# Optimization experiments

Measured on AMD Instinct MI355X. Metric: run time of the kernel, lower is better.

Reference implementation:

```python
import jax, jax.numpy as jnp
import numpy as np

C = 1024   # n_embd = dim_att = dim_k = dim_v
H = 16     # n_head
K = 64     # k_head_size
V = 64     # v_head_size
DF = 2048  # dim_ffn = (2*C)//32*32
B = 4
T = 1024
N_LAYER = 24
LAYER_ID = 12


def setup_inputs() -> dict:
    key = jax.random.key(0)
    ks = jax.random.split(key, 8)
    r01 = LAYER_ID / (N_LAYER - 1)
    r10 = 1.0 - LAYER_ID / N_LAYER
    ddd = (jnp.arange(C, dtype=jnp.float32) / C)[None, None, :]
    maa_x = 1.0 - ddd ** r10
    maa_k = 1.0 - ddd ** r10
    maa_v = 1.0 - (ddd ** r10 + 0.3 * r01)
    maa_r = 1.0 - ddd ** (0.5 * r10)
    n = jnp.arange(C, dtype=jnp.float32)
    zigzag = ((jnp.arange(C) + 1) % 3 - 1).astype(jnp.float32) * 0.1
    u = (r01 * (1.0 - n / (C - 1)) + zigzag).reshape(H, K)
    # LoRA mats: torch init is zeros / uniform(-0.01,0.01); use small uniform for both
    # so the token-shift LoRA path is actually exercised.
    w1 = jax.random.uniform(ks[0], (C, 96), minval=-0.01, maxval=0.01)
    w2 = jax.random.uniform(ks[1], (3, 32, C), minval=-0.01, maxval=0.01)
    s = 0.02
    Wr = jax.random.normal(ks[2], (C, C)) * s
    Wk = jax.random.normal(ks[3], (C, C)) * s
    Wvg = jax.random.normal(ks[4], (C, 2 * (C + DF))) * s
    Wo = jax.random.normal(ks[5], (C + DF, C)) * s
    ln_g = jnp.ones((C,), jnp.float32)
    ln_b = jnp.zeros((C,), jnp.float32)
    x = jax.random.normal(ks[6], (B, T, C), dtype=jnp.float32)
    return dict(x=x, maa_x=maa_x, maa_k=maa_k, maa_v=maa_v, maa_r=maa_r,
                w1=w1, w2=w2, u=u, Wr=Wr, Wk=Wk, Wvg=Wvg, Wo=Wo,
                ln_g=ln_g, ln_b=ln_b)


def _wkv6(r, k, v, e, u):
    # r,k,e: (B,T,H,K); v: (B,T,H,V); u: (H,K). Decayed linear-attention scan.
    rt = r.transpose(1, 0, 2, 3)
    kt = k.transpose(1, 0, 2, 3)
    vt = v.transpose(1, 0, 2, 3)
    et = e.transpose(1, 0, 2, 3)

    def step(S, inp):  # S: (B,H,K,V)
        r_t, k_t, v_t, e_t = inp
        kv = k_t[..., :, None] * v_t[..., None, :]           # (B,H,K,V)
        out = jnp.einsum('bhk,bhkv->bhv', r_t, S + u[None, :, :, None] * kv)
        return S * e_t[..., :, None] + kv, out

    S0 = jnp.zeros((r.shape[0], u.shape[0], u.shape[1], v.shape[-1]), r.dtype)
    _, o = jax.lax.scan(step, S0, (rt, kt, vt, et))
    return o.transpose(1, 0, 2, 3)  # (B,T,H,V)


def reference(x, maa_x, maa_k, maa_v, maa_r, w1, w2, u, Wr, Wk, Wvg, Wo, ln_g, ln_b):
    Bx, Tx, Cx = x.shape
    # time_shift: ZeroPad2d((0,0,1,-1)) -> shift right by 1 along T with zero pad
    xs = jnp.concatenate([jnp.zeros_like(x[:, :1]), x[:, :-1]], axis=1)
    xx = xs - x
    xxx = x + xx * maa_x
    m = jnp.tanh(xxx @ w1).reshape(Bx, Tx, 3, -1)        # (B,T,3,32)
    m = jnp.einsum('btld,ldc->lbtc', m, w2)              # (3,B,T,C)
    mk, mv, mr = m[0], m[1], m[2]
    xk = x + xx * (maa_k + mk)
    xv = x + xx * (maa_v + mv)
    xr = x + xx * (maa_r + mr)
    r = xr @ Wr
    w = xk @ Wk
    e = jnp.exp(-jnp.exp(w))   # per-channel decay used by the WKV kernel
    k = 1.0 - e                # k = 1 - exp(-exp(w))
    vg = xv @ Wvg
    vffn, gate = jnp.split(vg, 2, axis=-1)
    vffn = vffn * jax.nn.silu(gate)
    v, ffn = vffn[..., :Cx], vffn[..., Cx:]
    o = _wkv6(r.reshape(Bx, Tx, H, K), k.reshape(Bx, Tx, H, K),
              v.reshape(Bx, Tx, H, V), e.reshape(Bx, Tx, H, K), u)
    o = o.reshape(Bx, Tx, Cx)
    mu = o.mean(-1, keepdims=True)
    var = o.var(-1, keepdims=True)
    o = (o - mu) / jnp.sqrt(var + 1e-5) * ln_g + ln_b
    return jnp.concatenate([o, ffn], axis=-1) @ Wo
```

## Files before the change

kernel.cpp:

```cpp
#include <hip/hip_runtime.h>
#include <hip/hip_bf16.h>
#include <math.h>

#define Bn 4
#define Tn 1024
#define Cn 1024
#define Hn 16
#define Kn 64
#define DFn 2048
#define NCn 16
#define Ln 64

typedef __bf16 bf16x8 __attribute__((ext_vector_type(8)));
typedef float f32x4 __attribute__((ext_vector_type(4)));

#define GLD(dst, src) \
  __builtin_amdgcn_global_load_lds((__attribute__((address_space(1))) const void*)(src), \
                                   (__attribute__((address_space(3))) void*)(dst), 16, 0, 0)

__device__ __forceinline__ float rdlane(float v, int l) {
  return __int_as_float(__builtin_amdgcn_readlane(__float_as_int(v), l));
}

__device__ __forceinline__ unsigned short bfbits(float f) {
  union { __hip_bfloat16 h; unsigned short u; } cv;
  cv.h = __float2bfloat16(f);
  return cv.u;
}

__global__ __launch_bounds__(256) void k_setup(const float* __restrict__ w1,
                                               const float* __restrict__ w2,
                                               const float* __restrict__ Wr,
                                               const float* __restrict__ Wk,
                                               const float* __restrict__ Wvg,
                                               const float* __restrict__ Wo,
                                               const float* __restrict__ x,
                                               const float* __restrict__ maa_x,
                                               __hip_bfloat16* __restrict__ w1t,
                                               __hip_bfloat16* __restrict__ w2t,
                                               __hip_bfloat16* __restrict__ Wrt,
                                               __hip_bfloat16* __restrict__ Wkt,
                                               __hip_bfloat16* __restrict__ Wvgt,
                                               __hip_bfloat16* __restrict__ Wot,
                                               float* __restrict__ xx,
                                               __hip_bfloat16* __restrict__ xxx16) {
  int b = blockIdx.x;
  if (b >= 11456) {
    int idx = (b - 11456) * 256 + threadIdx.x;
    int c4 = idx & 255;
    int bt = idx >> 8;
    int t = bt & (Tn - 1);
    const float4* x4 = (const float4*)x;
    float4 xv = x4[idx];
    float4 xp;
    if (t > 0) xp = x4[idx - 256];
    else { xp.x = 0.f; xp.y = 0.f; xp.z = 0.f; xp.w = 0.f; }
    float4 d;
    d.x = xp.x - xv.x; d.y = xp.y - xv.y; d.z = xp.z - xv.z; d.w = xp.w - xv.w;
    float4 m = ((const float4*)maa_x)[c4];
    ushort4 o;
    o.x = bfbits(fmaf(d.x, m.x, xv.x));
    o.y = bfbits(fmaf(d.y, m.y, xv.y));
    o.z = bfbits(fmaf(d.z, m.z, xv.z));
    o.w = bfbits(fmaf(d.w, m.w, xv.w));
    ((float4*)xx)[idx] = d;
    ((ushort4*)xxx16)[idx] = o;
    return;
  }
  const float* W; __hip_bfloat16* Wt; int K, N, nx, rel;
  if (b < 96)        { W = w1;  Wt = w1t;  K = 1024; N = 96;   nx = 3;   rel = b; }
  else if (b < 192)  { int l = (b - 96) >> 5; rel = (b - 96) & 31;
                       W = w2 + l * 32768; Wt = w2t + l * 32768; K = 32; N = 1024; nx = 32; }
  else if (b < 1216) { W = Wr;  Wt = Wrt;  K = 1024; N = 1024; nx = 32;  rel = b - 192; }
  else if (b < 2240) { W = Wk;  Wt = Wkt;  K = 1024; N = 1024; nx = 32;  rel = b - 1216; }
  else if (b < 8384) { W = Wvg; Wt = Wvgt; K = 1024; N = 6144; nx = 192; rel = b - 2240; }
  else               { W = Wo;  Wt = Wot;  K = 3072; N = 1024; nx = 32;  rel = b - 8384; }
  int n0 = (rel % nx) * 32, k0 = (rel / nx) * 32;
  __shared__ float tile[32][33];
  int tid = threadIdx.x;
  int c = tid & 31, r = tid >> 5;
  #pragma unroll
  for (int i = 0; i < 4; ++i)
    tile[r + i * 8][c] = W[(size_t)(k0 + r + i * 8) * N + n0 + c];
  __syncthreads();
  #pragma unroll
  for (int i = 0; i < 4; ++i)
    Wt[(size_t)(n0 + r + i * 8) * K + k0 + c] = __float2bfloat16(tile[c][r + i * 8]);
}

__global__ __launch_bounds__(256) void k_mix1_16(const __hip_bfloat16* __restrict__ A,
                                                 const __hip_bfloat16* __restrict__ Bt,
                                                 __hip_bfloat16* __restrict__ m1) {
  const int K = 1024;
  __shared__ __align__(16) __hip_bfloat16 Al[128 * 32];
  __shared__ __align__(16) __hip_bfloat16 Bl[96 * 32];
  const int tid = threadIdx.x;
  const int wid = tid >> 6, lane = tid & 63;
  const int wr = wid >> 1, wc = wid & 1;
  const int row0 = blockIdx.x * 128;
  const char* gsrc[4];
  char* ldst[4];
  bool act[4];
  #pragma unroll
  for (int i = 0; i < 4; ++i) {
    const int s = i * 4 + wid;
    act[i] = (s < 14);
    const int ss = act[i] ? s : 0;
    if (ss < 8) {
      const int r = ss * 16 + (lane >> 2);
      gsrc[i] = (const char*)(A + (size_t)(row0 + r) * K) + (lane & 3) * 16;
      ldst[i] = (char*)&Al[0] + ss * 1024;
    } else {
      const int r = (ss - 8) * 16 + (lane >> 2);
      gsrc[i] = (const char*)(Bt + (size_t)r * K) + (lane & 3) * 16;
      ldst[i] = (char*)&Bl[0] + (ss - 8) * 1024;
    }
  }
  f32x4 acc[4][3];
  #pragma unroll
  for (int i = 0; i < 4; ++i)
    #pragma unroll
    for (int j = 0; j < 3; ++j)
      acc[i][j] = (f32x4){0.f, 0.f, 0.f, 0.f};
  const int g = lane >> 4, m = lane & 15;
  for (int k0 = 0; k0 < K; k0 += 32) {
    #pragma unroll
    for (int i = 0; i < 4; ++i) if (act[i]) GLD(ldst[i], gsrc[i]);
    #pragma unroll
    for (int i = 0; i < 4; ++i) gsrc[i] += 64;
    __syncthreads();
    bf16x8 af[4], bfr[3];
    #pragma unroll
    for (int i = 0; i < 4; ++i)
      af[i] = *(const bf16x8*)&Al[(wr * 64 + i * 16 + m) * 32 + g * 8];
    #pragma unroll
    for (int j = 0; j < 3; ++j)
      bfr[j] = *(const bf16x8*)&Bl[(wc * 48 + j * 16 + m) * 32 + g * 8];
    #pragma unroll
    for (int i = 0; i < 4; ++i)
      #pragma unroll
      for (int j = 0; j < 3; ++j)
        acc[i][j] = __builtin_amdgcn_mfma_f32_16x16x32_bf16(af[i], bfr[j], acc[i][j], 0, 0, 0);
    __syncthreads();
  }
  #pragma unroll
  for (int i = 0; i < 4; ++i) {
    const int grow = row0 + wr * 64 + i * 16 + g * 4;
    #pragma unroll
    for (int j = 0; j < 3; ++j) {
      const int gcol = wc * 48 + j * 16 + m;
      #pragma unroll
      for (int e = 0; e < 4; ++e)
        m1[(size_t)(grow + e) * 96 + gcol] = __float2bfloat16(tanhf(acc[i][j][e]));
    }
  }
}

__global__ __launch_bounds__(256) void k_mix2_16(const __hip_bfloat16* __restrict__ m1,
                                                 const __hip_bfloat16* __restrict__ w2t,
                                                 const float* __restrict__ x,
                                                 const float* __restrict__ xx,
                                                 const float* __restrict__ maa_k,
                                                 const float* __restrict__ maa_v,
                                                 const float* __restrict__ maa_r,
                                                 __hip_bfloat16* __restrict__ xk,
                                                 __hip_bfloat16* __restrict__ xv,
                                                 __hip_bfloat16* __restrict__ xr) {
  __shared__ __align__(16) __hip_bfloat16 Al[128 * 96];
  __shared__ __align__(16) __hip_bfloat16 Bl[3 * 64 * 32];
  const int tid = threadIdx.x;
  const int wid = tid >> 6, lane = tid & 63;
  const int wr = wid >> 1, wc = wid & 1;
  const int row0 = blockIdx.y * 128, col0 = blockIdx.x * 64;
  {
    const char* abase = (const char*)(m1 + (size_t)row0 * 96) + lane * 16;
    #pragma unroll
    for (int i = 0; i < 6; ++i) {
      const int s = wid + i * 4;
      GLD((char*)&Al[0] + s * 1024, abase + s * 1024);
    }
  }
  {
    const char* bbase = (const char*)w2t + (size_t)col0 * 64 + lane * 16;
    #pragma unroll
    for (int i = 0; i < 3; ++i) {
      const int s = wid + i * 4;
      const int l = s >> 2, q = s & 3;
      GLD((char*)&Bl[0] + s * 1024, bbase + (size_t)l * 65536 + q * 1024);
    }
  }
  __syncthreads();
  const int g = lane >> 4, m = lane & 15;
  f32x4 a0[4][2], a1[4][2], a2[4][2];
  #pragma unroll
  for (int i = 0; i < 4; ++i)
    #pragma unroll
    for (int j = 0; j < 2; ++j) {
      a0[i][j] = (f32x4){0.f,0.f,0.f,0.f};
      a1[i][j] = (f32x4){0.f,0.f,0.f,0.f};
      a2[i][j] = (f32x4){0.f,0.f,0.f,0.f};
    }
  #pragma unroll
  for (int l = 0; l < 3; ++l) {
    bf16x8 af[4], bfj[2];
    #pragma unroll
    for (int i = 0; i < 4; ++i)
      af[i] = *(const bf16x8*)&Al[(wr * 64 + i * 16 + m) * 96 + l * 32 + g * 8];
    #pragma unroll
    for (int j = 0; j < 2; ++j)
      bfj[j] = *(const bf16x8*)&Bl[(l * 64 + wc * 32 + j * 16 + m) * 32 + g * 8];
    #pragma unroll
    for (int i = 0; i < 4; ++i)
      #pragma unroll
      for (int j = 0; j < 2; ++j) {
        if (l == 0) a0[i][j] = __builtin_amdgcn_mfma_f32_16x16x32_bf16(af[i], bfj[j], a0[i][j], 0, 0, 0);
        if (l == 1) a1[i][j] = __builtin_amdgcn_mfma_f32_16x16x32_bf16(af[i], bfj[j], a1[i][j], 0, 0, 0);
        if (l == 2) a2[i][j] = __builtin_amdgcn_mfma_f32_16x16x32_bf16(af[i], bfj[j], a2[i][j], 0, 0, 0);
      }
  }
  #pragma unroll
  for (int i = 0; i < 4; ++i) {
    const int grow = row0 + wr * 64 + i * 16 + g * 4;
    #pragma unroll
    for (int j = 0; j < 2; ++j) {
      const int gcol = col0 + wc * 32 + j * 16 + m;
      const float mk_ = maa_k[gcol], mv_ = maa_v[gcol], mr_ = maa_r[gcol];
      #pragma unroll
      for (int e = 0; e < 4; ++e) {
        const size_t off = (size_t)(grow + e) * 1024 + gcol;
        const float xval = x[off], xxv = xx[off];
        xk[off] = __float2bfloat16(fmaf(xxv, mk_ + a0[i][j][e], xval));
        xv[off] = __float2bfloat16(fmaf(xxv, mv_ + a1[i][j][e], xval));
        xr[off] = __float2bfloat16(fmaf(xxv, mr_ + a2[i][j][e], xval));
      }
    }
  }
}

__global__ __launch_bounds__(256) void k_gemm_re(const __hip_bfloat16* __restrict__ Ar,
                                                 const __hip_bfloat16* __restrict__ Btr,
                                                 float* __restrict__ Cr,
                                                 const __hip_bfloat16* __restrict__ Ak,
                                                 const __hip_bfloat16* __restrict__ Btk,
                                                 float* __restrict__ Ck) {
  const int K = 1024, N = 1024;
  const int z = blockIdx.z;
  const __hip_bfloat16* A  = z ? Ak : Ar;
  const __hip_bfloat16* Bt = z ? Btk : Btr;
  float* C = z ? Ck : Cr;
  __shared__ __align__(16) __hip_bfloat16 Al[128 * 32];
  __shared__ __align__(16) __hip_bfloat16 Bl[64 * 32];
  const int tid = threadIdx.x;
  const int wid = tid >> 6, lane = tid & 63;
  const int wr = wid >> 1, wc = wid & 1;
  const int row0 = blockIdx.y * 128, col0 = blockIdx.x * 64;
  const char* gsrc[3];
  char* ldst[3];
  #pragma unroll
  for (int i = 0; i < 3; ++i) {
    const int s = wid + i * 4;
    if (s < 8) {
      const int r = s * 16 + (lane >> 2);
      gsrc[i] = (const char*)(A + (size_t)(row0 + r) * K) + (lane & 3) * 16;
      ldst[i] = (char*)&Al[0] + s * 1024;
    } else {
      const int r = (s - 8) * 16 + (lane >> 2);
      gsrc[i] = (const char*)(Bt + (size_t)(col0 + r) * K) + (lane & 3) * 16;
      ldst[i] = (char*)&Bl[0] + (s - 8) * 1024;
    }
  }
  f32x4 acc[4][2];
  #pragma unroll
  for (int i = 0; i < 4; ++i)
    #pragma unroll
    for (int j = 0; j < 2; ++j)
      acc[i][j] = (f32x4){0.f, 0.f, 0.f, 0.f};
  const int g = lane >> 4, m = lane & 15;
  for (int k0 = 0; k0 < K; k0 += 32) {
    #pragma unroll
    for (int i = 0; i < 3; ++i) GLD(ldst[i], gsrc[i]);
    #pragma unroll
    for (int i = 0; i < 3; ++i) gsrc[i] += 64;
    __syncthreads();
    bf16x8 af[4], bfr[2];
    #pragma unroll
    for (int i = 0; i < 4; ++i)
      af[i] = *(const bf16x8*)&Al[(wr * 64 + i * 16 + m) * 32 + g * 8];
    #pragma unroll
    for (int j = 0; j < 2; ++j)
      bfr[j] = *(const bf16x8*)&Bl[(wc * 32 + j * 16 + m) * 32 + g * 8];
    #pragma unroll
    for (int i = 0; i < 4; ++i)
      #pragma unroll
      for (int j = 0; j < 2; ++j)
        acc[i][j] = __builtin_amdgcn_mfma_f32_16x16x32_bf16(af[i], bfr[j], acc[i][j], 0, 0, 0);
    __syncthreads();
  }
  #pragma unroll
  for (int i = 0; i < 4; ++i) {
    const int grow = row0 + wr * 64 + i * 16 + g * 4;
    #pragma unroll
    for (int j = 0; j < 2; ++j) {
      const int gcol = col0 + wc * 32 + j * 16 + m;
      #pragma unroll
      for (int e = 0; e < 4; ++e) {
        float val = acc[i][j][e];
        if (z) val = expf(-expf(val));
        C[(size_t)(grow + e) * N + gcol] = val;
      }
    }
  }
}

__global__ __launch_bounds__(256) void k_gemm_vg16(const __hip_bfloat16* __restrict__ A,
                                                   const __hip_bfloat16* __restrict__ Bt,
                                                   float* __restrict__ v,
                                                   __hip_bfloat16* __restrict__ ffn) {
  const int K = 1024;
  __shared__ __align__(16) __hip_bfloat16 Al[128 * 32];
  __shared__ __align__(16) __hip_bfloat16 B1l[64 * 32];
  __shared__ __align__(16) __hip_bfloat16 B2l[64 * 32];
  const int tid = threadIdx.x;
  const int wid = tid >> 6, lane = tid & 63;
  const int wr = wid >> 1, wc = wid & 1;
  const int row0 = blockIdx.y * 128, col0 = blockIdx.x * 64;
  const char* gsrc[4];
  char* ldst[4];
  #pragma unroll
  for (int i = 0; i < 4; ++i) {
    const int s = wid + i * 4;
    if (s < 8) {
      const int r = s * 16 + (lane >> 2);
      gsrc[i] = (const char*)(A + (size_t)(row0 + r) * K) + (lane & 3) * 16;
      ldst[i] = (char*)&Al[0] + s * 1024;
    } else if (s < 12) {
      const int r = col0 + (s - 8) * 16 + (lane >> 2);
      gsrc[i] = (const char*)(Bt + (size_t)r * K) + (lane & 3) * 16;
      ldst[i] = (char*)&B1l[0] + (s - 8) * 1024;
    } else {
      const int r = 3072 + col0 + (s - 12) * 16 + (lane >> 2);
      gsrc[i] = (const char*)(Bt + (size_t)r * K) + (lane & 3) * 16;
      ldst[i] = (char*)&B2l[0] + (s - 12) * 1024;
    }
  }
  f32x4 a1[4][2], a2[4][2];
  #pragma unroll
  for (int i = 0; i < 4; ++i)
    #pragma unroll
    for (int j = 0; j < 2; ++j) {
      a1[i][j] = (f32x4){0.f, 0.f, 0.f, 0.f};
      a2[i][j] = (f32x4){0.f, 0.f, 0.f, 0.f};
    }
  const int g = lane >> 4, m = lane & 15;
  for (int k0 = 0; k0 < K; k0 += 32) {
    #pragma unroll
    for (int i = 0; i < 4; ++i) GLD(ldst[i], gsrc[i]);
    #pragma unroll
    for (int i = 0; i < 4; ++i) gsrc[i] += 64;
    __syncthreads();
    bf16x8 af[4], b1f[2], b2f[2];
    #pragma unroll
    for (int i = 0; i < 4; ++i)
      af[i] = *(const bf16x8*)&Al[(wr * 64 + i * 16 + m) * 32 + g * 8];
    #pragma unroll
    for (int j = 0; j < 2; ++j) {
      b1f[j] = *(const bf16x8*)&B1l[(wc * 32 + j * 16 + m) * 32 + g * 8];
      b2f[j] = *(const bf16x8*)&B2l[(wc * 32 + j * 16 + m) * 32 + g * 8];
    }
    #pragma unroll
    for (int i = 0; i < 4; ++i)
      #pragma unroll
      for (int j = 0; j < 2; ++j) {
        a1[i][j] = __builtin_amdgcn_mfma_f32_16x16x32_bf16(af[i], b1f[j], a1[i][j], 0, 0, 0);
        a2[i][j] = __builtin_amdgcn_mfma_f32_16x16x32_bf16(af[i], b2f[j], a2[i][j], 0, 0, 0);
      }
    __syncthreads();
  }
  const bool to_v = (col0 < 1024);
  #pragma unroll
  for (int i = 0; i < 4; ++i) {
    const int grow = row0 + wr * 64 + i * 16 + g * 4;
    #pragma unroll
    for (int j = 0; j < 2; ++j) {
      const int gcol = col0 + wc * 32 + j * 16 + m;
      #pragma unroll
      for (int e = 0; e < 4; ++e) {
        float gate = a2[i][j][e];
        float val = a1[i][j][e] * (gate / (1.f + expf(-gate)));
        if (to_v) v[(size_t)(grow + e) * 1024 + gcol] = val;
        else ffn[(size_t)(grow + e) * 2048 + (gcol - 1024)] = __float2bfloat16(val);
      }
    }
  }
}

__global__ __launch_bounds__(256) void k_gemm_wo16(const __hip_bfloat16* __restrict__ A1,
                                                   const __hip_bfloat16* __restrict__ A2,
                                                   const __hip_bfloat16* __restrict__ Bt,
                                                   float* __restrict__ C) {
  const int Kt = 3072;
  __shared__ __align__(16) __hip_bfloat16 Al[128 * 32];
  __shared__ __align__(16) __hip_bfloat16 Bl[64 * 32];
  const int tid = threadIdx.x;
  const int wid = tid >> 6, lane = tid & 63;
  const int wr = wid >> 1, wc = wid & 1;
  const int row0 = blockIdx.y * 128, col0 = blockIdx.x * 64;
  const char* gsrc[3];
  char* ldst[3];
  #pragma unroll
  for (int i = 0; i < 3; ++i) {
    const int s = wid + i * 4;
    if (s < 8) {
      const int r = s * 16 + (lane >> 2);
      gsrc[i] = (const char*)(A1 + (size_t)(row0 + r) * 1024) + (lane & 3) * 16;
      ldst[i] = (char*)&Al[0] + s * 1024;
    } else {
      const int r = col0 + (s - 8) * 16 + (lane >> 2);
      gsrc[i] = (const char*)(Bt + (size_t)r * Kt) + (lane & 3) * 16;
      ldst[i] = (char*)&Bl[0] + (s - 8) * 1024;
    }
  }
  f32x4 acc[4][2];
  #pragma unroll
  for (int i = 0; i < 4; ++i)
    #pragma unroll
    for (int j = 0; j < 2; ++j)
      acc[i][j] = (f32x4){0.f, 0.f, 0.f, 0.f};
  const int g = lane >> 4, m = lane & 15;

  #define WO_STEP() do {                                                          \
    _Pragma("unroll")                                                             \
    for (int i = 0; i < 3; ++i) GLD(ldst[i], gsrc[i]);                            \
    _Pragma("unroll")                                                             \
    for (int i = 0; i < 3; ++i) gsrc[i] += 64;                                    \
    __syncthreads();                                                              \
    bf16x8 af[4], bfr[2];                                                         \
    _Pragma("unroll")                                                             \
    for (int i = 0; i < 4; ++i)                                                   \
      af[i] = *(const bf16x8*)&Al[(wr * 64 + i * 16 + m) * 32 + g * 8];           \
    _Pragma("unroll")                                                             \
    for (int j = 0; j < 2; ++j)                                                   \
      bfr[j] = *(const bf16x8*)&Bl[(wc * 32 + j * 16 + m) * 32 + g * 8];          \
    _Pragma("unroll")                                                             \
    for (int i = 0; i < 4; ++i)                                                   \
      _Pragma("unroll")                                                           \
      for (int j = 0; j < 2; ++j)                                                 \
        acc[i][j] = __builtin_amdgcn_mfma_f32_16x16x32_bf16(af[i], bfr[j],        \
                                                            acc[i][j], 0, 0, 0); \
    __syncthreads();                                                              \
  } while (0)

  for (int k0 = 0; k0 < 1024; k0 += 32) WO_STEP();
  #pragma unroll
  for (int i = 0; i < 3; ++i) {
    const int s = wid + i * 4;
    if (s < 8) {
      const int r = s * 16 + (lane >> 2);
      gsrc[i] = (const char*)(A2 + (size_t)(row0 + r) * 2048) + (lane & 3) * 16;
    }
  }
  for (int k0 = 0; k0 < 2048; k0 += 32) WO_STEP();
  #undef WO_STEP

  #pragma unroll
  for (int i = 0; i < 4; ++i) {
    const int grow = row0 + wr * 64 + i * 16 + g * 4;
    #pragma unroll
    for (int j = 0; j < 2; ++j) {
      const int gcol = col0 + wc * 32 + j * 16 + m;
      #pragma unroll
      for (int e = 0; e < 4; ++e)
        C[(size_t)(grow + e) * 1024 + gcol] = acc[i][j][e];
    }
  }
}

#define TTn 8
__global__ __launch_bounds__(256) void k_wkv1(const float* __restrict__ r,
                                              const float* __restrict__ e,
                                              const float* __restrict__ v,
                                              const float* __restrict__ u,
                                              float* __restrict__ o,
                                              float* __restrict__ Dcum,
                                              float* __restrict__ Dtot,
                                              float* __restrict__ Inc) {
  int blk = blockIdx.x;
  int c = blk & (NCn - 1);
  int bh = blk >> 4;
  int b = bh >> 4, h = bh & 15;
  int tid = threadIdx.x, wave = tid >> 6, lane = tid & 63;
  size_t base = (size_t)b * Tn * Cn + (size_t)h * 64 + (size_t)c * Ln * Cn;
  int jbase = wave * 16 + (lane & 15);
  float uv = u[h * 64 + jbase];
  float st[16];
  #pragma unroll
  for (int i = 0; i < 16; ++i) st[i] = 0.f;
  float cum = 1.f;
  __shared__ float yp[4][TTn][64];
  for (int tb = 0; tb < Ln / TTn; ++tb) {
    float rv8[TTn], ev8[TTn], vv8[TTn];
    #pragma unroll
    for (int tt = 0; tt < TTn; ++tt) {
      size_t off = base + (size_t)(tb * TTn + tt) * Cn;
      rv8[tt] = r[off + jbase];
      ev8[tt] = e[off + jbase];
      vv8[tt] = v[off + lane];
    }
    float yb[TTn];
    #pragma unroll
    for (int tt = 0; tt < TTn; ++tt) {
      const float rv = rv8[tt], ev = ev8[tt], vv = vv8[tt];
      if (lane < 16)
        Dcum[base + (size_t)(tb * TTn + tt) * Cn + jbase] = cum;
      cum *= ev;
      float p = rv * uv * (1.f - ev);
      p += __shfl_xor(p, 1, 16);
      p += __shfl_xor(p, 2, 16);
      p += __shfl_xor(p, 4, 16);
      p += __shfl_xor(p, 8, 16);
      float y = p * vv;
      #pragma unroll
      for (int jj = 0; jj < 16; ++jj) {
        float rj = rdlane(rv, jj);
        float ej = rdlane(ev, jj);
        float kv = fmaf(-ej, vv, vv);
        y = fmaf(rj, st[jj], y);
        st[jj] = fmaf(st[jj], ej, kv);
      }
      yb[tt] = y;
    }
    #pragma unroll
    for (int tt = 0; tt < TTn; ++tt) yp[wave][tt][lane] = yb[tt];
    __syncthreads();
    #pragma unroll
    for (int q = 0; q < TTn / 4; ++q) {
      int tt = wave * (TTn / 4) + q;
      size_t off = base + (size_t)(tb * TTn + tt) * Cn;
      o[off + lane] = yp[0][tt][lane] + yp[1][tt][lane] + yp[2][tt][lane] + yp[3][tt][lane];
    }
    __syncthreads();
  }
  size_t sbase = ((size_t)bh * NCn + c) * 4096;
  #pragma unroll
  for (int jj = 0; jj < 16; ++jj)
    Inc[sbase + (size_t)(wave * 16 + jj) * 64 + lane] = st[jj];
  if (lane < 16)
    Dtot[((size_t)bh * NCn + c) * 64 + jbase] = cum;
}

__global__ __launch_bounds__(256) void k_wkv2(float* __restrict__ S,
                                              const float* __restrict__ Dtot) {
  int bh = blockIdx.x;
  int tid = threadIdx.x;
  float4 s[4];
  #pragma unroll
  for (int j = 0; j < 4; ++j) { s[j].x = 0.f; s[j].y = 0.f; s[j].z = 0.f; s[j].w = 0.f; }
  size_t sb = (size_t)bh * NCn * 4096;
  for (int c = 0; c < NCn; ++c) {
    float4* entry = (float4*)(S + sb + (size_t)c * 4096);
    const float* dt = Dtot + ((size_t)bh * NCn + c) * 64;
    #pragma unroll
    for (int j = 0; j < 4; ++j) {
      int idx4 = tid + j * 256;
      int k = idx4 >> 4;
      float d = dt[k];
      float4 inc = entry[idx4];
      float4 cur = s[j];
      entry[idx4] = cur;
      s[j].x = fmaf(cur.x, d, inc.x);
      s[j].y = fmaf(cur.y, d, inc.y);
      s[j].z = fmaf(cur.z, d, inc.z);
      s[j].w = fmaf(cur.w, d, inc.w);
    }
  }
}

__global__ __launch_bounds__(256) void k_wkv3(const float* __restrict__ r,
                                              const float* __restrict__ Dcum,
                                              const float* __restrict__ S,
                                              float* __restrict__ o) {
  int blk = blockIdx.x;
  int c = blk & (NCn - 1);
  if (c == 0) return;
  int bh = blk >> 4;
  int b = bh >> 4, h = bh & 15;
  int tid = threadIdx.x, wave = tid >> 6, lane = tid & 63;
  const float* Sg = S + ((size_t)bh * NCn + c) * 4096;
  float sreg[64];
  #pragma unroll
  for (int k = 0; k < 64; ++k) sreg[k] = Sg[k * 64 + lane];
  size_t base = (size_t)b * Tn * Cn + (size_t)h * 64 + (size_t)c * Ln * Cn;
  for (int ti = 0; ti < 16; ++ti) {
    int t = wave * 16 + ti;
    size_t off = base + (size_t)t * Cn;
    float rd = r[off + lane] * Dcum[off + lane];
    float y = 0.f;
    #pragma unroll
    for (int k = 0; k < 64; ++k)
      y = fmaf(rdlane(rd, k), sreg[k], y);
    o[off + lane] += y;
  }
}

__global__ __launch_bounds__(256) void k_ln(const float* __restrict__ o,
                                            const float* __restrict__ g,
                                            const float* __restrict__ bta,
                                            __hip_bfloat16* __restrict__ ln16) {
  int bt = blockIdx.x, tid = threadIdx.x;
  const float4* row = (const float4*)(o + (size_t)bt * 1024);
  float4 v = row[tid];
  float s = v.x + v.y + v.z + v.w;
  float s2 = fmaf(v.x, v.x, fmaf(v.y, v.y, fmaf(v.z, v.z, v.w * v.w)));
  #pragma unroll
  for (int m = 1; m < 64; m <<= 1) {
    s += __shfl_xor(s, m, 64);
    s2 += __shfl_xor(s2, m, 64);
  }
  __shared__ float rs[4], rq[4];
  if ((tid & 63) == 0) { rs[tid >> 6] = s; rq[tid >> 6] = s2; }
  __syncthreads();
  s = rs[0] + rs[1] + rs[2] + rs[3];
  s2 = rq[0] + rq[1] + rq[2] + rq[3];
  float mu = s * (1.f / 1024.f);
  float var = s2 * (1.f / 1024.f) - mu * mu;
  float rstd = rsqrtf(var + 1e-5f);
  float4 gv = ((const float4*)g)[tid];
  float4 bv = ((const float4*)bta)[tid];
  ushort4 outv;
  outv.x = bfbits(fmaf((v.x - mu) * rstd, gv.x, bv.x));
  outv.y = bfbits(fmaf((v.y - mu) * rstd, gv.y, bv.y));
  outv.z = bfbits(fmaf((v.z - mu) * rstd, gv.z, bv.z));
  outv.w = bfbits(fmaf((v.w - mu) * rstd, gv.w, bv.w));
  ((ushort4*)((unsigned short*)ln16 + (size_t)bt * 1024))[tid] = outv;
}

extern "C" void kernel_launch(void* const* d_in, const int* in_sizes, int n_in,
                              void* d_out, int out_size, void* d_ws, size_t ws_size,
                              hipStream_t stream) {
  const float* x     = (const float*)d_in[0];
  const float* maa_x = (const float*)d_in[1];
  const float* maa_k = (const float*)d_in[2];
  const float* maa_v = (const float*)d_in[3];
  const float* maa_r = (const float*)d_in[4];
  const float* w1    = (const float*)d_in[5];
  const float* w2    = (const float*)d_in[6];
  const float* u     = (const float*)d_in[7];
  const float* Wr    = (const float*)d_in[8];
  const float* Wk    = (const float*)d_in[9];
  const float* Wvg   = (const float*)d_in[10];
  const float* Wo    = (const float*)d_in[11];
  const float* ln_g  = (const float*)d_in[12];
  const float* ln_b  = (const float*)d_in[13];
  float* out = (float*)d_out;
  float* ws = (float*)d_ws;

  const size_t M1 = 1048576;
  float* xx    = ws;
  __hip_bfloat16* xxx16 = (__hip_bfloat16*)(ws + 4 * M1);
  __hip_bfloat16* m1_16 = (__hip_bfloat16*)(ws + 8 * M1);
  __hip_bfloat16* w1t = (__hip_bfloat16*)(ws + 8 * M1 + 393216);
  __hip_bfloat16* w2t = (__hip_bfloat16*)(ws + 8 * M1 + 442368);
  __hip_bfloat16* xk16 = (__hip_bfloat16*)(ws + 8 * M1 + 524288);
  __hip_bfloat16* xv16 = (__hip_bfloat16*)(ws + 10 * M1 + 524288);
  __hip_bfloat16* xr16 = (__hip_bfloat16*)(ws + 12 * M1 + 524288);
  float* ee    = ws + 14 * M1 + 524288;
  float* vv    = ws + 18 * M1 + 524288;
  float* Sbuf  = ws + 22 * M1 + 524288;
  __hip_bfloat16* ffn16 = (__hip_bfloat16*)(ws + 26 * M1 + 524288);
  __hip_bfloat16* Wr16t = (__hip_bfloat16*)(ws + 30 * M1 + 524288);
  __hip_bfloat16* Wk16t = (__hip_bfloat16*)(ws + 31 * M1);
  __hip_bfloat16* Wvg16t = (__hip_bfloat16*)(ws + 31 * M1 + 524288);
  __hip_bfloat16* Wo16t = (__hip_bfloat16*)(ws + 34 * M1 + 524288);
  float* rr = ws + 4 * M1;
  float* oo = xx;
  float* Dcum = ws + 8 * M1 + 524288;
  float* Dtot = (float*)m1_16;
  __hip_bfloat16* ln16 = (__hip_bfloat16*)Sbuf;

  k_setup<<<15552, 256, 0, stream>>>(w1, w2, Wr, Wk, Wvg, Wo, x, maa_x,
                                     w1t, w2t, Wr16t, Wk16t, Wvg16t, Wo16t,
                                     xx, xxx16);
  k_mix1_16<<<32, 256, 0, stream>>>(xxx16, w1t, m1_16);
  k_mix2_16<<<dim3(16, 32), 256, 0, stream>>>(m1_16, w2t, x, xx, maa_k, maa_v, maa_r,
                                              xk16, xv16, xr16);
  k_gemm_re<<<dim3(16, 32, 2), 256, 0, stream>>>(xr16, Wr16t, rr, xk16, Wk16t, ee);
  k_gemm_vg16<<<dim3(48, 32), 256, 0, stream>>>(xv16, Wvg16t, vv, ffn16);
  k_wkv1<<<64 * NCn, 256, 0, stream>>>(rr, ee, vv, u, oo, Dcum, Dtot, Sbuf);
  k_wkv2<<<64, 256, 0, stream>>>(Sbuf, Dtot);
  k_wkv3<<<64 * NCn, 256, 0, stream>>>(rr, Dcum, Sbuf, oo);
  k_ln<<<4096, 256, 0, stream>>>(oo, ln_g, ln_b, ln16);
  k_gemm_wo16<<<dim3(16, 32), 256, 0, stream>>>(ln16, ffn16, Wo16t, out);
}
```

Measured before the change: 322.8 us.

## Merge r/k and vg GEMMs into one launch; load wkv scalars via uniform loads

The separate r/k GEMM and value-gate GEMM launches are combined into a single 2560-block kernel that picks its sub-problem from the block index. This removes one launch and the tail gap between the two GEMMs, letting both sets of tiles share the GPU at once. In the wkv1 scan, the per-step readlane broadcasts of r and e are replaced by loads through a wave-uniform address, which the compiler can turn into scalar loads that take VALU pressure off the inner loop. The risks are extra scalar-memory latency in the serial recurrence, and an uneven mix of block sizes in the merged grid.

```diff
diff --git a/kernel.cpp b/kernel.cpp
--- a/kernel.cpp
+++ b/kernel.cpp
@@ -237,93 +237,92 @@
   }
 }
 
-__global__ __launch_bounds__(256) void k_gemm_re(const __hip_bfloat16* __restrict__ Ar,
-                                                 const __hip_bfloat16* __restrict__ Btr,
-                                                 float* __restrict__ Cr,
-                                                 const __hip_bfloat16* __restrict__ Ak,
-                                                 const __hip_bfloat16* __restrict__ Btk,
-                                                 float* __restrict__ Ck) {
-  const int K = 1024, N = 1024;
-  const int z = blockIdx.z;
-  const __hip_bfloat16* A  = z ? Ak : Ar;
-  const __hip_bfloat16* Bt = z ? Btk : Btr;
-  float* C = z ? Ck : Cr;
-  __shared__ __align__(16) __hip_bfloat16 Al[128 * 32];
-  __shared__ __align__(16) __hip_bfloat16 Bl[64 * 32];
-  const int tid = threadIdx.x;
-  const int wid = tid >> 6, lane = tid & 63;
-  const int wr = wid >> 1, wc = wid & 1;
-  const int row0 = blockIdx.y * 128, col0 = blockIdx.x * 64;
-  const char* gsrc[3];
-  char* ldst[3];
-  #pragma unroll
-  for (int i = 0; i < 3; ++i) {
-    const int s = wid + i * 4;
-    if (s < 8) {
-      const int r = s * 16 + (lane >> 2);
-      gsrc[i] = (const char*)(A + (size_t)(row0 + r) * K) + (lane & 3) * 16;
-      ldst[i] = (char*)&Al[0] + s * 1024;
-    } else {
-      const int r = (s - 8) * 16 + (lane >> 2);
-      gsrc[i] = (const char*)(Bt + (size_t)(col0 + r) * K) + (lane & 3) * 16;
-      ldst[i] = (char*)&Bl[0] + (s - 8) * 1024;
-    }
-  }
-  f32x4 acc[4][2];
-  #pragma unroll
-  for (int i = 0; i < 4; ++i)
-    #pragma unroll
-    for (int j = 0; j < 2; ++j)
-      acc[i][j] = (f32x4){0.f, 0.f, 0.f, 0.f};
-  const int g = lane >> 4, m = lane & 15;
-  for (int k0 = 0; k0 < K; k0 += 32) {
-    #pragma unroll
-    for (int i = 0; i < 3; ++i) GLD(ldst[i], gsrc[i]);
-    #pragma unroll
-    for (int i = 0; i < 3; ++i) gsrc[i] += 64;
-    __syncthreads();
-    bf16x8 af[4], bfr[2];
-    #pragma unroll
-    for (int i = 0; i < 4; ++i)
-      af[i] = *(const bf16x8*)&Al[(wr * 64 + i * 16 + m) * 32 + g * 8];
-    #pragma unroll
-    for (int j = 0; j < 2; ++j)
-      bfr[j] = *(const bf16x8*)&Bl[(wc * 32 + j * 16 + m) * 32 + g * 8];
-    #pragma unroll
-    for (int i = 0; i < 4; ++i)
-      #pragma unroll
-      for (int j = 0; j < 2; ++j)
-        acc[i][j] = __builtin_amdgcn_mfma_f32_16x16x32_bf16(af[i], bfr[j], acc[i][j], 0, 0, 0);
-    __syncthreads();
-  }
-  #pragma unroll
-  for (int i = 0; i < 4; ++i) {
-    const int grow = row0 + wr * 64 + i * 16 + g * 4;
-    #pragma unroll
-    for (int j = 0; j < 2; ++j) {
-      const int gcol = col0 + wc * 32 + j * 16 + m;
-      #pragma unroll
-      for (int e = 0; e < 4; ++e) {
-        float val = acc[i][j][e];
-        if (z) val = expf(-expf(val));
-        C[(size_t)(grow + e) * N + gcol] = val;
-      }
-    }
-  }
-}
-
-__global__ __launch_bounds__(256) void k_gemm_vg16(const __hip_bfloat16* __restrict__ A,
-                                                   const __hip_bfloat16* __restrict__ Bt,
-                                                   float* __restrict__ v,
-                                                   __hip_bfloat16* __restrict__ ffn) {
+__global__ __launch_bounds__(256) void k_gemm_rev(const __hip_bfloat16* __restrict__ xr,
+                                                  const __hip_bfloat16* __restrict__ Wrt,
+                                                  float* __restrict__ rr,
+                                                  const __hip_bfloat16* __restrict__ xk,
+                                                  const __hip_bfloat16* __restrict__ Wkt,
+                                                  float* __restrict__ ee,
+                                                  const __hip_bfloat16* __restrict__ xv,
+                                                  const __hip_bfloat16* __restrict__ Wvgt,
+                                                  float* __restrict__ vv,
+                                                  __hip_bfloat16* __restrict__ ffn) {
   const int K = 1024;
   __shared__ __align__(16) __hip_bfloat16 Al[128 * 32];
   __shared__ __align__(16) __hip_bfloat16 B1l[64 * 32];
   __shared__ __align__(16) __hip_bfloat16 B2l[64 * 32];
+  const int b = blockIdx.x;
   const int tid = threadIdx.x;
   const int wid = tid >> 6, lane = tid & 63;
   const int wr = wid >> 1, wc = wid & 1;
-  const int row0 = blockIdx.y * 128, col0 = blockIdx.x * 64;
+  const int g = lane >> 4, m = lane & 15;
+
+  if (b < 1024) {
+    const int z = b >> 9;
+    const int idx = b & 511;
+    const int row0 = (idx >> 4) * 128, col0 = (idx & 15) * 64;
+    const __hip_bfloat16* A  = z ? xk : xr;
+    const __hip_bfloat16* Bt = z ? Wkt : Wrt;
+    float* C = z ? ee : rr;
+    const char* gsrc[3];
+    char* ldst[3];
+    #pragma unroll
+    for (int i = 0; i < 3; ++i) {
+      const int s = wid + i * 4;
+      if (s < 8) {
+        const int r = s * 16 + (lane >> 2);
+        gsrc[i] = (const char*)(A + (size_t)(row0 + r) * K) + (lane & 3) * 16;
+        ldst[i] = (char*)&Al[0] + s * 1024;
+      } else {
+        const int r = (s - 8) * 16 + (lane >> 2);
+        gsrc[i] = (const char*)(Bt + (size_t)(col0 + r) * K) + (lane & 3) * 16;
+        ldst[i] = (char*)&B1l[0] + (s - 8) * 1024;
+      }
+    }
+    f32x4 acc[4][2];
+    #pragma unroll
+    for (int i = 0; i < 4; ++i)
+      #pragma unroll
+      for (int j = 0; j < 2; ++j)
+        acc[i][j] = (f32x4){0.f, 0.f, 0.f, 0.f};
+    for (int k0 = 0; k0 < K; k0 += 32) {
+      #pragma unroll
+      for (int i = 0; i < 3; ++i) GLD(ldst[i], gsrc[i]);
+      #pragma unroll
+      for (int i = 0; i < 3; ++i) gsrc[i] += 64;
+      __syncthreads();
+      bf16x8 af[4], bfr[2];
+      #pragma unroll
+      for (int i = 0; i < 4; ++i)
+        af[i] = *(const bf16x8*)&Al[(wr * 64 + i * 16 + m) * 32 + g * 8];
+      #pragma unroll
+      for (int j = 0; j < 2; ++j)
+        bfr[j] = *(const bf16x8*)&B1l[(wc * 32 + j * 16 + m) * 32 + g * 8];
+      #pragma unroll
+      for (int i = 0; i < 4; ++i)
+        #pragma unroll
+        for (int j = 0; j < 2; ++j)
+          acc[i][j] = __builtin_amdgcn_mfma_f32_16x16x32_bf16(af[i], bfr[j], acc[i][j], 0, 0, 0);
+      __syncthreads();
+    }
+    #pragma unroll
+    for (int i = 0; i < 4; ++i) {
+      const int grow = row0 + wr * 64 + i * 16 + g * 4;
+      #pragma unroll
+      for (int j = 0; j < 2; ++j) {
+        const int gcol = col0 + wc * 32 + j * 16 + m;
+        #pragma unroll
+        for (int e = 0; e < 4; ++e) {
+          float val = acc[i][j][e];
+          if (z) val = expf(-expf(val));
+          C[(size_t)(grow + e) * 1024 + gcol] = val;
+        }
+      }
+    }
+    return;
+  }
+  const int rel = b - 1024;
+  const int row0 = (rel / 48) * 128, col0 = (rel % 48) * 64;
   const char* gsrc[4];
   char* ldst[4];
   #pragma unroll
@@ -331,15 +330,15 @@
     const int s = wid + i * 4;
     if (s < 8) {
       const int r = s * 16 + (lane >> 2);
-      gsrc[i] = (const char*)(A + (size_t)(row0 + r) * K) + (lane & 3) * 16;
+      gsrc[i] = (const char*)(xv + (size_t)(row0 + r) * K) + (lane & 3) * 16;
       ldst[i] = (char*)&Al[0] + s * 1024;
     } else if (s < 12) {
       const int r = col0 + (s - 8) * 16 + (lane >> 2);
-      gsrc[i] = (const char*)(Bt + (size_t)r * K) + (lane & 3) * 16;
+      gsrc[i] = (const char*)(Wvgt + (size_t)r * K) + (lane & 3) * 16;
       ldst[i] = (char*)&B1l[0] + (s - 8) * 1024;
     } else {
       const int r = 3072 + col0 + (s - 12) * 16 + (lane >> 2);
-      gsrc[i] = (const char*)(Bt + (size_t)r * K) + (lane & 3) * 16;
+      gsrc[i] = (const char*)(Wvgt + (size_t)r * K) + (lane & 3) * 16;
       ldst[i] = (char*)&B2l[0] + (s - 12) * 1024;
     }
   }
@@ -351,7 +350,6 @@
       a1[i][j] = (f32x4){0.f, 0.f, 0.f, 0.f};
       a2[i][j] = (f32x4){0.f, 0.f, 0.f, 0.f};
     }
-  const int g = lane >> 4, m = lane & 15;
   for (int k0 = 0; k0 < K; k0 += 32) {
     #pragma unroll
     for (int i = 0; i < 4; ++i) GLD(ldst[i], gsrc[i]);
@@ -387,7 +385,7 @@
       for (int e = 0; e < 4; ++e) {
         float gate = a2[i][j][e];
         float val = a1[i][j][e] * (gate / (1.f + expf(-gate)));
-        if (to_v) v[(size_t)(grow + e) * 1024 + gcol] = val;
+        if (to_v) vv[(size_t)(grow + e) * 1024 + gcol] = val;
         else ffn[(size_t)(grow + e) * 2048 + (gcol - 1024)] = __float2bfloat16(val);
       }
     }
@@ -491,6 +489,8 @@
   int tid = threadIdx.x, wave = tid >> 6, lane = tid & 63;
   size_t base = (size_t)b * Tn * Cn + (size_t)h * 64 + (size_t)c * Ln * Cn;
   int jbase = wave * 16 + (lane & 15);
+  const int wu = __builtin_amdgcn_readfirstlane(wave);
+  const size_t ubase = base + (size_t)wu * 16;
   float uv = u[h * 64 + jbase];
   float st[16];
   #pragma unroll
@@ -519,11 +519,13 @@
       p += __shfl_xor(p, 4, 16);
       p += __shfl_xor(p, 8, 16);
       float y = p * vv;
+      const float* rrow = r + ubase + (size_t)(tb * TTn + tt) * Cn;
+      const float* erow = e + ubase + (size_t)(tb * TTn + tt) * Cn;
       #pragma unroll
       for (int jj = 0; jj < 16; ++jj) {
-        float rj = rdlane(rv, jj);
-        float ej = rdlane(ev, jj);
-        float kv = fmaf(-ej, vv, vv);
+        const float rj = rrow[jj];
+        const float ej = erow[jj];
+        const float kv = fmaf(-ej, vv, vv);
         y = fmaf(rj, st[jj], y);
         st[jj] = fmaf(st[jj], ej, kv);
       }
@@ -683,8 +685,8 @@
   k_mix1_16<<<32, 256, 0, stream>>>(xxx16, w1t, m1_16);
   k_mix2_16<<<dim3(16, 32), 256, 0, stream>>>(m1_16, w2t, x, xx, maa_k, maa_v, maa_r,
                                               xk16, xv16, xr16);
-  k_gemm_re<<<dim3(16, 32, 2), 256, 0, stream>>>(xr16, Wr16t, rr, xk16, Wk16t, ee);
-  k_gemm_vg16<<<dim3(48, 32), 256, 0, stream>>>(xv16, Wvg16t, vv, ffn16);
+  k_gemm_rev<<<2560, 256, 0, stream>>>(xr16, Wr16t, rr, xk16, Wk16t, ee,
+                                       xv16, Wvg16t, vv, ffn16);
   k_wkv1<<<64 * NCn, 256, 0, stream>>>(rr, ee, vv, u, oo, Dcum, Dtot, Sbuf);
   k_wkv2<<<64, 256, 0, stream>>>(Sbuf, Dtot);
   k_wkv3<<<64 * NCn, 256, 0, stream>>>(rr, Dcum, Sbuf, oo);
```

After: 321.6 us. Within noise of the previous version (-0.4%).
